# Kernel tuning notes

Hardware: AMD Instinct MI355X
Metric: run time of the kernel (lower is better)

Reference implementation:

```python
import jax, jax.numpy as jnp
import numpy as np

E = 16          # num_experts
TOP_K = 4       # num_experts_per_tok
H = 2048        # hidden_size
I_MOE = 1408    # moe_intermediate_size
I_SH = 5632     # shared_expert_intermediate_size
NORM_TOPK = False


def setup_inputs() -> dict:
    key = jax.random.key(0)
    ks = jax.random.split(key, 9)
    s = 0.02  # init scale
    return {
        "hidden_states": jax.random.normal(ks[0], (1, 1024, H), jnp.float32),
        "w_router": jax.random.normal(ks[1], (E, H), jnp.float32) * s,        # gate.weight [E,H]
        "w_gate": jax.random.normal(ks[2], (E, I_MOE, H), jnp.float32) * s,   # per-expert gate_proj.weight
        "w_up": jax.random.normal(ks[3], (E, I_MOE, H), jnp.float32) * s,     # per-expert up_proj.weight
        "w_down": jax.random.normal(ks[4], (E, H, I_MOE), jnp.float32) * s,   # per-expert down_proj.weight
        "ws_gate": jax.random.normal(ks[5], (I_SH, H), jnp.float32) * s,      # shared expert gate_proj
        "ws_up": jax.random.normal(ks[6], (I_SH, H), jnp.float32) * s,        # shared expert up_proj
        "ws_down": jax.random.normal(ks[7], (H, I_SH), jnp.float32) * s,      # shared expert down_proj
        "w_shared_gate": jax.random.normal(ks[8], (1, H), jnp.float32) * s,   # shared_expert_gate.weight
    }


def reference(hidden_states, w_router, w_gate, w_up, w_down,
              ws_gate, ws_up, ws_down, w_shared_gate):
    B, S, Hd = hidden_states.shape
    x = hidden_states.reshape(-1, Hd)                       # [T,H]
    T = x.shape[0]

    # router
    router_logits = x @ w_router.T                          # [T,E]
    probs = jax.nn.softmax(router_logits.astype(jnp.float32), axis=-1)
    topk_w, topk_idx = jax.lax.top_k(probs, TOP_K)          # [T,K]
    if NORM_TOPK:
        topk_w = topk_w / topk_w.sum(axis=-1, keepdims=True)
    topk_w = topk_w.astype(x.dtype)

    # dense combine weights: comb[t,e] = routing weight of expert e for token t (0 if unselected)
    comb = jnp.zeros((T, E), x.dtype).at[jnp.arange(T)[:, None], topk_idx].add(topk_w)

    # experts: SiLU-gated MLP, weighted combine (zero weight => no contribution)
    g = jax.nn.silu(jnp.einsum('th,eih->eti', x, w_gate)) * jnp.einsum('th,eih->eti', x, w_up)  # [E,T,I]
    moe_out = jnp.einsum('eti,ehi,te->th', g, w_down, comb)  # [T,H]

    # shared expert with sigmoid gate
    sh = (jax.nn.silu(x @ ws_gate.T) * (x @ ws_up.T)) @ ws_down.T   # [T,H]
    sh = jax.nn.sigmoid(x @ w_shared_gate.T) * sh

    final = (moe_out + sh).reshape(B, S, Hd)
    return final, router_logits
```

## Files before the change

kernel.cpp:

```cpp
#include <hip/hip_runtime.h>
#include <hip/hip_bf16.h>
#include <cmath>

#define TT   1024
#define HH   2048
#define EE   16
#define KTOP 4
#define IM   1408
#define ISHD 5632
#define BK   64

typedef __bf16 bf16x8 __attribute__((ext_vector_type(8)));
typedef __bf16 bf16x4 __attribute__((ext_vector_type(4)));
typedef float  f32x4  __attribute__((ext_vector_type(4)));

__device__ inline bf16x4 cvt4(float4 f) {
    bf16x4 r;
    r[0] = (__bf16)f.x; r[1] = (__bf16)f.y; r[2] = (__bf16)f.z; r[3] = (__bf16)f.w;
    return r;
}

__device__ inline void lds_dma16(void* lds, const void* g) {
    __builtin_amdgcn_global_load_lds(
        (const __attribute__((address_space(1))) unsigned int*)g,
        (__attribute__((address_space(3))) unsigned int*)lds, 16, 0, 0);
}

__global__ __launch_bounds__(256) void cvtx_kernel(
    const float* __restrict__ x, __bf16* __restrict__ xb) {
    const int i = (blockIdx.x * 256 + threadIdx.x) * 4;
    *(bf16x4*)(xb + i) = cvt4(*(const float4*)(x + i));
}

__global__ __launch_bounds__(256) void router_kernel(
    const float* __restrict__ x, const float* __restrict__ wr,
    const float* __restrict__ wshg,
    float* __restrict__ out_logits, int* __restrict__ counts,
    int* __restrict__ topk_e, int* __restrict__ topk_slot,
    float* __restrict__ topk_w, float* __restrict__ sgate)
{
    const int t    = blockIdx.x;
    const int tid  = threadIdx.x;
    const int wave = tid >> 6;
    const int lane = tid & 63;

    __shared__ float logits[EE];
    __shared__ float sgv;

    const float* xrow = x + (size_t)t * HH;
    float4 xv[4][2];
#pragma unroll
    for (int c = 0; c < 4; c++) {
        xv[c][0] = *(const float4*)(xrow + c * 512 + lane * 8);
        xv[c][1] = *(const float4*)(xrow + c * 512 + lane * 8 + 4);
    }

#pragma unroll
    for (int j = 0; j < 4; j++) {
        const int e = wave * 4 + j;
        const float* wrow = wr + (size_t)e * HH;
        float s = 0.f;
#pragma unroll
        for (int c = 0; c < 4; c++) {
            float4 w0 = *(const float4*)(wrow + c * 512 + lane * 8);
            float4 w1 = *(const float4*)(wrow + c * 512 + lane * 8 + 4);
            s += xv[c][0].x * w0.x + xv[c][0].y * w0.y + xv[c][0].z * w0.z + xv[c][0].w * w0.w;
            s += xv[c][1].x * w1.x + xv[c][1].y * w1.y + xv[c][1].z * w1.z + xv[c][1].w * w1.w;
        }
        for (int off = 32; off > 0; off >>= 1) s += __shfl_down(s, off, 64);
        if (lane == 0) logits[e] = s;
    }
    if (wave == 0) {
        float s = 0.f;
#pragma unroll
        for (int c = 0; c < 4; c++) {
            float4 w0 = *(const float4*)(wshg + c * 512 + lane * 8);
            float4 w1 = *(const float4*)(wshg + c * 512 + lane * 8 + 4);
            s += xv[c][0].x * w0.x + xv[c][0].y * w0.y + xv[c][0].z * w0.z + xv[c][0].w * w0.w;
            s += xv[c][1].x * w1.x + xv[c][1].y * w1.y + xv[c][1].z * w1.z + xv[c][1].w * w1.w;
        }
        for (int off = 32; off > 0; off >>= 1) s += __shfl_down(s, off, 64);
        if (lane == 0) sgv = s;
    }
    __syncthreads();

    if (tid == 0) {
        float mx = -1e30f;
        for (int e = 0; e < EE; e++) {
            out_logits[t * EE + e] = logits[e];
            mx = fmaxf(mx, logits[e]);
        }
        float p[EE]; float den = 0.f;
        for (int e = 0; e < EE; e++) { p[e] = expf(logits[e] - mx); den += p[e]; }
        const float inv = 1.f / den;
        bool used[EE];
        for (int e = 0; e < EE; e++) used[e] = false;
        for (int k = 0; k < KTOP; k++) {
            int best = 0; float bv = -1.f;
            for (int e = 0; e < EE; e++)
                if (!used[e] && p[e] > bv) { bv = p[e]; best = e; }
            used[best] = true;
            int slot = atomicAdd(&counts[best], 1);
            topk_e[t * KTOP + k]    = best;
            topk_slot[t * KTOP + k] = slot;
            topk_w[t * KTOP + k]    = bv * inv;
        }
        sgate[t] = 1.f / (1.f + expf(-sgv));
    }
}

__global__ void scan_kernel(const int* __restrict__ counts,
                            int* __restrict__ offsets) {
    if (threadIdx.x == 0 && blockIdx.x == 0) {
        int a = 0;
        for (int e = 0; e < EE; e++) { offsets[e] = a; a += counts[e]; }
        offsets[EE] = a;
    }
}

__global__ __launch_bounds__(256) void scatter_kernel(
    const int* __restrict__ offsets, const int* __restrict__ topk_e,
    const int* __restrict__ topk_slot, const float* __restrict__ topk_w,
    int* __restrict__ tok_list, float* __restrict__ wlist)
{
    const int i = blockIdx.x * 256 + threadIdx.x;
    if (i < TT * KTOP) {
        const int e   = topk_e[i];
        const int pos = offsets[e] + topk_slot[i];
        tok_list[pos] = i >> 2;
        wlist[pos]    = topk_w[i];
    }
}

__global__ __launch_bounds__(256) void gateup_kernel(
    const __bf16* __restrict__ xb, const float* __restrict__ wgate,
    const float* __restrict__ wup, const int* __restrict__ counts,
    const int* __restrict__ offsets, const int* __restrict__ tok_list,
    const float* __restrict__ wlist, __bf16* __restrict__ Gout, const int I)
{
    const int e    = blockIdx.z;
    const int Ne   = counts ? counts[e]  : TT;
    const int base = counts ? offsets[e] : 0;
    const int m0 = blockIdx.y * 128;
    if (m0 >= Ne) return;
    const int n0 = blockIdx.x * 64;

    __shared__ __bf16 As[2][128][64];
    __shared__ __bf16 Bgs[2][64][64];
    __shared__ __bf16 Bus[2][64][64];

    const int tid  = threadIdx.x;
    const int wave = tid >> 6, lane = tid & 63;

    const int arw = lane >> 3;
    const int sc8 = ((lane & 7) ^ arw) * 8;
    const __bf16* agp[4];
#pragma unroll
    for (int p = 0; p < 4; p++) {
        const int row = p * 32 + wave * 8 + arw;
        const int sc  = min(m0 + row, Ne - 1);
        const int tok = tok_list ? tok_list[base + sc] : sc;
        agp[p] = xb + (size_t)tok * HH + sc8;
    }

    const int brow = tid >> 4;
    const int bc4  = tid & 15;
    const float* bgptr[4];
    const float* buptr[4];
#pragma unroll
    for (int p = 0; p < 4; p++) {
        const size_t off = ((size_t)e * I + n0 + p * 16 + brow) * HH + bc4 * 4;
        bgptr[p] = wgate + off;
        buptr[p] = wup   + off;
    }
    const int bwo = ((((bc4 >> 1) ^ (brow & 7)) << 3) | ((bc4 & 1) << 2));

    const int wm = wave >> 1, wn = wave & 1;
    const int q = lane >> 4, r = lane & 15;
    const int r7 = r & 7;

    f32x4 accg[4][2], accu[4][2];
#pragma unroll
    for (int i = 0; i < 4; i++)
#pragma unroll
        for (int j = 0; j < 2; j++) {
            accg[i][j] = (f32x4){0.f, 0.f, 0.f, 0.f};
            accu[i][j] = (f32x4){0.f, 0.f, 0.f, 0.f};
        }

    float4 bgv[4], buv[4];

    auto loadB = [&](int kk) {
#pragma unroll
        for (int p = 0; p < 4; p++) {
            bgv[p] = *(const float4*)(bgptr[p] + kk);
            buv[p] = *(const float4*)(buptr[p] + kk);
        }
    };
    auto writeB = [&](int buf) {
#pragma unroll
        for (int p = 0; p < 4; p++) {
            *(bf16x4*)&Bgs[buf][p * 16 + brow][bwo] = cvt4(bgv[p]);
            *(bf16x4*)&Bus[buf][p * 16 + brow][bwo] = cvt4(buv[p]);
        }
    };
    auto issueA = [&](int buf, int kk) {
#pragma unroll
        for (int p = 0; p < 4; p++)
            lds_dma16(&As[buf][p * 32 + wave * 8][0], agp[p] + kk);
    };
    auto compute = [&](int buf) {
#pragma unroll
        for (int ks = 0; ks < BK; ks += 32) {
            const int cb = (ks >> 3) + q;
            bf16x8 af[4], bgf[2], buf2[2];
#pragma unroll
            for (int i = 0; i < 4; i++)
                af[i] = *(const bf16x8*)&As[buf][wm * 64 + i * 16 + r][(cb ^ r7) * 8];
#pragma unroll
            for (int j = 0; j < 2; j++) {
                bgf[j]  = *(const bf16x8*)&Bgs[buf][wn * 32 + j * 16 + r][(cb ^ r7) * 8];
                buf2[j] = *(const bf16x8*)&Bus[buf][wn * 32 + j * 16 + r][(cb ^ r7) * 8];
            }
#pragma unroll
            for (int i = 0; i < 4; i++)
#pragma unroll
                for (int j = 0; j < 2; j++) {
                    accg[i][j] = __builtin_amdgcn_mfma_f32_16x16x32_bf16(af[i], bgf[j],  accg[i][j], 0, 0, 0);
                    accu[i][j] = __builtin_amdgcn_mfma_f32_16x16x32_bf16(af[i], buf2[j], accu[i][j], 0, 0, 0);
                }
        }
    };

    constexpr int NS = HH / BK;
    loadB(0);
    issueA(0, 0);
    writeB(0);
    loadB(BK);
    for (int s = 0; s < NS; ++s) {
        __syncthreads();
        const int cur = s & 1;
        if (s + 1 < NS) {
            writeB(cur ^ 1);
            issueA(cur ^ 1, (s + 1) * BK);
            if (s + 2 < NS) loadB((s + 2) * BK);
        }
        compute(cur);
    }

#pragma unroll
    for (int i = 0; i < 4; i++)
#pragma unroll
        for (int reg = 0; reg < 4; reg++) {
            const int srow = m0 + wm * 64 + i * 16 + q * 4 + reg;
            if (srow < Ne) {
                const float w = wlist ? wlist[base + srow] : 1.f;
                __bf16* gp = Gout + (size_t)(base + srow) * I + n0 + wn * 32;
#pragma unroll
                for (int j = 0; j < 2; j++) {
                    float g = accg[i][j][reg];
                    float u = accu[i][j][reg];
                    float act = g / (1.f + expf(-g));
                    gp[j * 16 + r] = (__bf16)(act * u * w);
                }
            }
        }
}

__global__ __launch_bounds__(256) void down_kernel(
    const __bf16* __restrict__ G, const float* __restrict__ wd,
    const int* __restrict__ counts, const int* __restrict__ offsets,
    const int* __restrict__ tok_list, float* __restrict__ moeacc)
{
    const int e    = blockIdx.z;
    const int Ne   = counts[e];
    const int base = offsets[e];
    const int m0 = blockIdx.y * 128;
    if (m0 >= Ne) return;
    const int n0 = blockIdx.x * 128;

    __shared__ __bf16 As[2][128][64];
    __shared__ __bf16 Bs[2][128][64];

    const int tid  = threadIdx.x;
    const int wave = tid >> 6, lane = tid & 63;

    const int arw = lane >> 3;
    const int sc8 = ((lane & 7) ^ arw) * 8;
    const __bf16* agp[4];
#pragma unroll
    for (int p = 0; p < 4; p++) {
        const int row = p * 32 + wave * 8 + arw;
        const int sc  = min(m0 + row, Ne - 1);
        agp[p] = G + (size_t)(base + sc) * IM + sc8;
    }

    const int brow = tid >> 4;
    const int bc4  = tid & 15;
    const float* bptr[8];
#pragma unroll
    for (int p = 0; p < 8; p++)
        bptr[p] = wd + ((size_t)e * HH + n0 + p * 16 + brow) * IM + bc4 * 4;
    const int bwo = ((((bc4 >> 1) ^ (brow & 7)) << 3) | ((bc4 & 1) << 2));

    const int wm = wave >> 1, wn = wave & 1;
    const int q = lane >> 4, r = lane & 15;
    const int r7 = r & 7;

    f32x4 acc[4][4];
#pragma unroll
    for (int i = 0; i < 4; i++)
#pragma unroll
        for (int j = 0; j < 4; j++) acc[i][j] = (f32x4){0.f, 0.f, 0.f, 0.f};

    float4 bv[8];

    auto loadB = [&](int kk) {
#pragma unroll
        for (int p = 0; p < 8; p++) bv[p] = *(const float4*)(bptr[p] + kk);
    };
    auto writeB = [&](int buf) {
#pragma unroll
        for (int p = 0; p < 8; p++)
            *(bf16x4*)&Bs[buf][p * 16 + brow][bwo] = cvt4(bv[p]);
    };
    auto issueA = [&](int buf, int kk) {
#pragma unroll
        for (int p = 0; p < 4; p++)
            lds_dma16(&As[buf][p * 32 + wave * 8][0], agp[p] + kk);
    };
    auto compute = [&](int buf) {
#pragma unroll
        for (int ks = 0; ks < BK; ks += 32) {
            const int cb = (ks >> 3) + q;
            bf16x8 af[4], bf[4];
#pragma unroll
            for (int i = 0; i < 4; i++)
                af[i] = *(const bf16x8*)&As[buf][wm * 64 + i * 16 + r][(cb ^ r7) * 8];
#pragma unroll
            for (int j = 0; j < 4; j++)
                bf[j] = *(const bf16x8*)&Bs[buf][wn * 64 + j * 16 + r][(cb ^ r7) * 8];
#pragma unroll
            for (int i = 0; i < 4; i++)
#pragma unroll
                for (int j = 0; j < 4; j++)
                    acc[i][j] = __builtin_amdgcn_mfma_f32_16x16x32_bf16(af[i], bf[j], acc[i][j], 0, 0, 0);
        }
    };

    constexpr int NS = IM / BK;
    loadB(0);
    issueA(0, 0);
    writeB(0);
    loadB(BK);
    for (int s = 0; s < NS; ++s) {
        __syncthreads();
        const int cur = s & 1;
        if (s + 1 < NS) {
            writeB(cur ^ 1);
            issueA(cur ^ 1, (s + 1) * BK);
            if (s + 2 < NS) loadB((s + 2) * BK);
        }
        compute(cur);
    }

#pragma unroll
    for (int i = 0; i < 4; i++)
#pragma unroll
        for (int reg = 0; reg < 4; reg++) {
            const int srow = m0 + wm * 64 + i * 16 + q * 4 + reg;
            if (srow < Ne) {
                const int tok = tok_list[base + srow];
                float* mp = moeacc + (size_t)tok * HH + n0 + wn * 64;
#pragma unroll
                for (int j = 0; j < 4; j++)
                    atomicAdd(mp + j * 16 + r, acc[i][j][reg]);
            }
        }
}

__global__ __launch_bounds__(256) void shdown_kernel(
    const __bf16* __restrict__ S, const float* __restrict__ wsd,
    const float* __restrict__ moeacc, const float* __restrict__ sgate,
    float* __restrict__ out)
{
    const int m0 = blockIdx.y * 128;
    const int n0 = blockIdx.x * 64;

    __shared__ __bf16 As[2][128][64];
    __shared__ __bf16 Bs[2][64][64];

    const int tid  = threadIdx.x;
    const int wave = tid >> 6, lane = tid & 63;

    const int arw = lane >> 3;
    const int sc8 = ((lane & 7) ^ arw) * 8;
    const __bf16* agp[4];
#pragma unroll
    for (int p = 0; p < 4; p++) {
        const int row = p * 32 + wave * 8 + arw;
        agp[p] = S + (size_t)(m0 + row) * ISHD + sc8;
    }

    const int brow = tid >> 4;
    const int bc4  = tid & 15;
    const float* bptr[4];
#pragma unroll
    for (int p = 0; p < 4; p++)
        bptr[p] = wsd + (size_t)(n0 + p * 16 + brow) * ISHD + bc4 * 4;
    const int bwo = ((((bc4 >> 1) ^ (brow & 7)) << 3) | ((bc4 & 1) << 2));

    const int wm = wave >> 1, wn = wave & 1;
    const int q = lane >> 4, r = lane & 15;
    const int r7 = r & 15 & 7;

    f32x4 acc[4][2];
#pragma unroll
    for (int i = 0; i < 4; i++)
#pragma unroll
        for (int j = 0; j < 2; j++) acc[i][j] = (f32x4){0.f, 0.f, 0.f, 0.f};

    float4 bv[4];

    auto loadB = [&](int kk) {
#pragma unroll
        for (int p = 0; p < 4; p++) bv[p] = *(const float4*)(bptr[p] + kk);
    };
    auto writeB = [&](int buf) {
#pragma unroll
        for (int p = 0; p < 4; p++)
            *(bf16x4*)&Bs[buf][p * 16 + brow][bwo] = cvt4(bv[p]);
    };
    auto issueA = [&](int buf, int kk) {
#pragma unroll
        for (int p = 0; p < 4; p++)
            lds_dma16(&As[buf][p * 32 + wave * 8][0], agp[p] + kk);
    };
    auto compute = [&](int buf) {
#pragma unroll
        for (int ks = 0; ks < BK; ks += 32) {
            const int cb = (ks >> 3) + q;
            bf16x8 af[4], bf[2];
#pragma unroll
            for (int i = 0; i < 4; i++)
                af[i] = *(const bf16x8*)&As[buf][wm * 64 + i * 16 + r][(cb ^ r7) * 8];
#pragma unroll
            for (int j = 0; j < 2; j++)
                bf[j] = *(const bf16x8*)&Bs[buf][wn * 32 + j * 16 + r][(cb ^ r7) * 8];
#pragma unroll
            for (int i = 0; i < 4; i++)
#pragma unroll
                for (int j = 0; j < 2; j++)
                    acc[i][j] = __builtin_amdgcn_mfma_f32_16x16x32_bf16(af[i], bf[j], acc[i][j], 0, 0, 0);
        }
    };

    constexpr int NS = ISHD / BK;
    loadB(0);
    issueA(0, 0);
    writeB(0);
    loadB(BK);
    for (int s = 0; s < NS; ++s) {
        __syncthreads();
        const int cur = s & 1;
        if (s + 1 < NS) {
            writeB(cur ^ 1);
            issueA(cur ^ 1, (s + 1) * BK);
            if (s + 2 < NS) loadB((s + 2) * BK);
        }
        compute(cur);
    }

#pragma unroll
    for (int i = 0; i < 4; i++)
#pragma unroll
        for (int reg = 0; reg < 4; reg++) {
            const int t  = m0 + wm * 64 + i * 16 + q * 4 + reg;
            const float sg = sgate[t];
            const float* mp = moeacc + (size_t)t * HH + n0 + wn * 32;
            float* op = out + (size_t)t * HH + n0 + wn * 32;
#pragma unroll
            for (int j = 0; j < 2; j++)
                op[j * 16 + r] = mp[j * 16 + r] + sg * acc[i][j][reg];
        }
}

extern "C" void kernel_launch(void* const* d_in, const int* in_sizes, int n_in,
                              void* d_out, int out_size, void* d_ws, size_t ws_size,
                              hipStream_t stream) {
    const float* x    = (const float*)d_in[0];
    const float* wr   = (const float*)d_in[1];
    const float* wg   = (const float*)d_in[2];
    const float* wu   = (const float*)d_in[3];
    const float* wd   = (const float*)d_in[4];
    const float* wsg  = (const float*)d_in[5];
    const float* wsu  = (const float*)d_in[6];
    const float* wsd  = (const float*)d_in[7];
    const float* wshg = (const float*)d_in[8];

    float* out        = (float*)d_out;
    float* out_logits = out + (size_t)TT * HH;

    char* ws = (char*)d_ws;
    int*    counts    = (int*)(ws + 0);
    int*    offsets   = (int*)(ws + 256);
    int*    topk_e    = (int*)(ws + 512);
    int*    topk_slot = (int*)(ws + 512 + 16384);
    float*  topk_w    = (float*)(ws + 512 + 32768);
    float*  sgate     = (float*)(ws + 512 + 49152);
    int*    tok_list  = (int*)(ws + 512 + 53248);
    float*  wlist     = (float*)(ws + 512 + 69632);
    __bf16* xb        = (__bf16*)(ws + 86528);
    float*  moeacc    = (float*)(ws + 86528 + 4194304);
    char*   GS        = (char*)moeacc + (size_t)TT * HH * 4;
    __bf16* G = (__bf16*)GS;
    __bf16* S = (__bf16*)GS;

    hipMemsetAsync(counts, 0, EE * sizeof(int), stream);
    hipMemsetAsync(moeacc, 0, (size_t)TT * HH * sizeof(float), stream);

    cvtx_kernel<<<TT * HH / 1024, 256, 0, stream>>>(x, xb);
    router_kernel<<<TT, 256, 0, stream>>>(x, wr, wshg, out_logits,
                                          counts, topk_e, topk_slot, topk_w, sgate);
    scan_kernel<<<1, 64, 0, stream>>>(counts, offsets);
    scatter_kernel<<<(TT * KTOP + 255) / 256, 256, 0, stream>>>(
        offsets, topk_e, topk_slot, topk_w, tok_list, wlist);

    gateup_kernel<<<dim3(IM / 64, TT / 128, EE), 256, 0, stream>>>(
        xb, wg, wu, counts, offsets, tok_list, wlist, G, IM);

    down_kernel<<<dim3(HH / 128, TT / 128, EE), 256, 0, stream>>>(
        G, wd, counts, offsets, tok_list, moeacc);

    gateup_kernel<<<dim3(ISHD / 64, TT / 128, 1), 256, 0, stream>>>(
        xb, wsg, wsu, nullptr, nullptr, nullptr, nullptr, S, ISHD);

    shdown_kernel<<<dim3(HH / 64, TT / 128, 1), 256, 0, stream>>>(
        S, wsd, moeacc, sgate, out);
}
```

Before: 996.3 us.

## Remap workgroups XCD-aware and deepen B-prefetch pipeline with explicit waitcnt barriers

Switches all four GEMM kernels to a 1D grid and remaps block IDs so that consecutive workgroups dispatched round-robin across the 8 XCDs land on neighbouring tiles. M-tiles of one N-tile share a chip's L2, which improves weight reuse. It also unrolls the main loop by two with two register sets of fp32 B prefetch, keeping loads two stages ahead. __syncthreads is replaced with manual s_waitcnt vmcnt plus s_barrier. The risks are more register pressure and fragile hand-counted vmcnt values that must match the number of outstanding loads.

```diff
diff --git a/kernel.cpp b/kernel.cpp
--- a/kernel.cpp
+++ b/kernel.cpp
@@ -25,6 +25,9 @@
         (const __attribute__((address_space(1))) unsigned int*)g,
         (__attribute__((address_space(3))) unsigned int*)lds, 16, 0, 0);
 }
+
+#define WAITCNT(vm) asm volatile("s_waitcnt vmcnt(" #vm ") lgkmcnt(0)" ::: "memory")
+#define BARRIER() do { __builtin_amdgcn_s_barrier(); __builtin_amdgcn_sched_barrier(0); } while (0)
 
 __global__ __launch_bounds__(256) void cvtx_kernel(
     const float* __restrict__ x, __bf16* __restrict__ xb) {
@@ -138,12 +141,21 @@
     const int* __restrict__ offsets, const int* __restrict__ tok_list,
     const float* __restrict__ wlist, __bf16* __restrict__ Gout, const int I)
 {
-    const int e    = blockIdx.z;
+    const int nwg   = gridDim.x;
+    const int chunk = nwg >> 3;
+    const int bid   = blockIdx.x;
+    const int orig  = (bid & 7) * chunk + (bid >> 3);
+    const int mt    = orig & 7;
+    const int rest  = orig >> 3;
+    const int NX    = I >> 6;
+    const int nt    = rest % NX;
+    const int e     = rest / NX;
+
     const int Ne   = counts ? counts[e]  : TT;
     const int base = counts ? offsets[e] : 0;
-    const int m0 = blockIdx.y * 128;
+    const int m0 = mt * 128;
     if (m0 >= Ne) return;
-    const int n0 = blockIdx.x * 64;
+    const int n0 = nt * 64;
 
     __shared__ __bf16 As[2][128][64];
     __shared__ __bf16 Bgs[2][64][64];
@@ -188,20 +200,34 @@
             accu[i][j] = (f32x4){0.f, 0.f, 0.f, 0.f};
         }
 
-    float4 bgv[4], buv[4];
-
-    auto loadB = [&](int kk) {
+    float4 bgv0[4], buv0[4], bgv1[4], buv1[4];
+
+    auto loadB0 = [&](int kk) {
 #pragma unroll
         for (int p = 0; p < 4; p++) {
-            bgv[p] = *(const float4*)(bgptr[p] + kk);
-            buv[p] = *(const float4*)(buptr[p] + kk);
-        }
-    };
-    auto writeB = [&](int buf) {
+            bgv0[p] = *(const float4*)(bgptr[p] + kk);
+            buv0[p] = *(const float4*)(buptr[p] + kk);
+        }
+    };
+    auto loadB1 = [&](int kk) {
 #pragma unroll
         for (int p = 0; p < 4; p++) {
-            *(bf16x4*)&Bgs[buf][p * 16 + brow][bwo] = cvt4(bgv[p]);
-            *(bf16x4*)&Bus[buf][p * 16 + brow][bwo] = cvt4(buv[p]);
+            bgv1[p] = *(const float4*)(bgptr[p] + kk);
+            buv1[p] = *(const float4*)(buptr[p] + kk);
+        }
+    };
+    auto writeB0 = [&](int buf) {
+#pragma unroll
+        for (int p = 0; p < 4; p++) {
+            *(bf16x4*)&Bgs[buf][p * 16 + brow][bwo] = cvt4(bgv0[p]);
+            *(bf16x4*)&Bus[buf][p * 16 + brow][bwo] = cvt4(buv0[p]);
+        }
+    };
+    auto writeB1 = [&](int buf) {
+#pragma unroll
+        for (int p = 0; p < 4; p++) {
+            *(bf16x4*)&Bgs[buf][p * 16 + brow][bwo] = cvt4(bgv1[p]);
+            *(bf16x4*)&Bus[buf][p * 16 + brow][bwo] = cvt4(buv1[p]);
         }
     };
     auto issueA = [&](int buf, int kk) {
@@ -233,19 +259,29 @@
     };
 
     constexpr int NS = HH / BK;
-    loadB(0);
-    issueA(0, 0);
-    writeB(0);
-    loadB(BK);
-    for (int s = 0; s < NS; ++s) {
-        __syncthreads();
-        const int cur = s & 1;
+    loadB0(0); issueA(0, 0);
+    writeB0(0);
+    loadB1(BK);
+    loadB0(2 * BK);
+    WAITCNT(16);
+    BARRIER();
+
+#pragma unroll 1
+    for (int s = 0; s < NS; s += 2) {
+        if (s + 1 < NS) { writeB1(1); issueA(1, (s + 1) * BK); }
+        if (s + 3 < NS) loadB1((s + 3) * BK);
+        compute(0);
         if (s + 1 < NS) {
-            writeB(cur ^ 1);
-            issueA(cur ^ 1, (s + 1) * BK);
-            if (s + 2 < NS) loadB((s + 2) * BK);
-        }
-        compute(cur);
+            if (s + 3 < NS) WAITCNT(8); else WAITCNT(0);
+            BARRIER();
+            if (s + 2 < NS) { writeB0(0); issueA(0, (s + 2) * BK); }
+            if (s + 4 < NS) loadB0((s + 4) * BK);
+            compute(1);
+            if (s + 2 < NS) {
+                if (s + 4 < NS) WAITCNT(8); else WAITCNT(0);
+                BARRIER();
+            }
+        }
     }
 
 #pragma unroll
@@ -272,12 +308,20 @@
     const int* __restrict__ counts, const int* __restrict__ offsets,
     const int* __restrict__ tok_list, float* __restrict__ moeacc)
 {
-    const int e    = blockIdx.z;
+    const int nwg   = gridDim.x;
+    const int chunk = nwg >> 3;
+    const int bid   = blockIdx.x;
+    const int orig  = (bid & 7) * chunk + (bid >> 3);
+    const int mt    = orig & 7;
+    const int rest  = orig >> 3;
+    const int nt    = rest & 15;
+    const int e     = rest >> 4;
+
     const int Ne   = counts[e];
     const int base = offsets[e];
-    const int m0 = blockIdx.y * 128;
+    const int m0 = mt * 128;
     if (m0 >= Ne) return;
-    const int n0 = blockIdx.x * 128;
+    const int n0 = nt * 128;
 
     __shared__ __bf16 As[2][128][64];
     __shared__ __bf16 Bs[2][128][64];
@@ -313,16 +357,25 @@
 #pragma unroll
         for (int j = 0; j < 4; j++) acc[i][j] = (f32x4){0.f, 0.f, 0.f, 0.f};
 
-    float4 bv[8];
-
-    auto loadB = [&](int kk) {
-#pragma unroll
-        for (int p = 0; p < 8; p++) bv[p] = *(const float4*)(bptr[p] + kk);
-    };
-    auto writeB = [&](int buf) {
+    float4 bv0[8], bv1[8];
+
+    auto loadB0 = [&](int kk) {
+#pragma unroll
+        for (int p = 0; p < 8; p++) bv0[p] = *(const float4*)(bptr[p] + kk);
+    };
+    auto loadB1 = [&](int kk) {
+#pragma unroll
+        for (int p = 0; p < 8; p++) bv1[p] = *(const float4*)(bptr[p] + kk);
+    };
+    auto writeB0 = [&](int buf) {
 #pragma unroll
         for (int p = 0; p < 8; p++)
-            *(bf16x4*)&Bs[buf][p * 16 + brow][bwo] = cvt4(bv[p]);
+            *(bf16x4*)&Bs[buf][p * 16 + brow][bwo] = cvt4(bv0[p]);
+    };
+    auto writeB1 = [&](int buf) {
+#pragma unroll
+        for (int p = 0; p < 8; p++)
+            *(bf16x4*)&Bs[buf][p * 16 + brow][bwo] = cvt4(bv1[p]);
     };
     auto issueA = [&](int buf, int kk) {
 #pragma unroll
@@ -349,19 +402,29 @@
     };
 
     constexpr int NS = IM / BK;
-    loadB(0);
-    issueA(0, 0);
-    writeB(0);
-    loadB(BK);
-    for (int s = 0; s < NS; ++s) {
-        __syncthreads();
-        const int cur = s & 1;
+    loadB0(0); issueA(0, 0);
+    writeB0(0);
+    loadB1(BK);
+    loadB0(2 * BK);
+    WAITCNT(16);
+    BARRIER();
+
+#pragma unroll 1
+    for (int s = 0; s < NS; s += 2) {
+        if (s + 1 < NS) { writeB1(1); issueA(1, (s + 1) * BK); }
+        if (s + 3 < NS) loadB1((s + 3) * BK);
+        compute(0);
         if (s + 1 < NS) {
-            writeB(cur ^ 1);
-            issueA(cur ^ 1, (s + 1) * BK);
-            if (s + 2 < NS) loadB((s + 2) * BK);
-        }
-        compute(cur);
+            if (s + 3 < NS) WAITCNT(8); else WAITCNT(0);
+            BARRIER();
+            if (s + 2 < NS) { writeB0(0); issueA(0, (s + 2) * BK); }
+            if (s + 4 < NS) loadB0((s + 4) * BK);
+            compute(1);
+            if (s + 2 < NS) {
+                if (s + 4 < NS) WAITCNT(8); else WAITCNT(0);
+                BARRIER();
+            }
+        }
     }
 
 #pragma unroll
@@ -384,8 +447,15 @@
     const float* __restrict__ moeacc, const float* __restrict__ sgate,
     float* __restrict__ out)
 {
-    const int m0 = blockIdx.y * 128;
-    const int n0 = blockIdx.x * 64;
+    const int nwg   = gridDim.x;
+    const int chunk = nwg >> 3;
+    const int bid   = blockIdx.x;
+    const int orig  = (bid & 7) * chunk + (bid >> 3);
+    const int mt    = orig & 7;
+    const int nt    = orig >> 3;
+
+    const int m0 = mt * 128;
+    const int n0 = nt * 64;
 
     __shared__ __bf16 As[2][128][64];
     __shared__ __bf16 Bs[2][64][64];
@@ -412,7 +482,7 @@
 
     const int wm = wave >> 1, wn = wave & 1;
     const int q = lane >> 4, r = lane & 15;
-    const int r7 = r & 15 & 7;
+    const int r7 = r & 7;
 
     f32x4 acc[4][2];
 #pragma unroll
@@ -420,16 +490,25 @@
 #pragma unroll
         for (int j = 0; j < 2; j++) acc[i][j] = (f32x4){0.f, 0.f, 0.f, 0.f};
 
-    float4 bv[4];
-
-    auto loadB = [&](int kk) {
-#pragma unroll
-        for (int p = 0; p < 4; p++) bv[p] = *(const float4*)(bptr[p] + kk);
-    };
-    auto writeB = [&](int buf) {
+    float4 bv0[4], bv1[4];
+
+    auto loadB0 = [&](int kk) {
+#pragma unroll
+        for (int p = 0; p < 4; p++) bv0[p] = *(const float4*)(bptr[p] + kk);
+    };
+    auto loadB1 = [&](int kk) {
+#pragma unroll
+        for (int p = 0; p < 4; p++) bv1[p] = *(const float4*)(bptr[p] + kk);
+    };
+    auto writeB0 = [&](int buf) {
 #pragma unroll
         for (int p = 0; p < 4; p++)
-            *(bf16x4*)&Bs[buf][p * 16 + brow][bwo] = cvt4(bv[p]);
+            *(bf16x4*)&Bs[buf][p * 16 + brow][bwo] = cvt4(bv0[p]);
+    };
+    auto writeB1 = [&](int buf) {
+#pragma unroll
+        for (int p = 0; p < 4; p++)
+            *(bf16x4*)&Bs[buf][p * 16 + brow][bwo] = cvt4(bv1[p]);
     };
     auto issueA = [&](int buf, int kk) {
 #pragma unroll
@@ -456,19 +535,29 @@
     };
 
     constexpr int NS = ISHD / BK;
-    loadB(0);
-    issueA(0, 0);
-    writeB(0);
-    loadB(BK);
-    for (int s = 0; s < NS; ++s) {
-        __syncthreads();
-        const int cur = s & 1;
+    loadB0(0); issueA(0, 0);
+    writeB0(0);
+    loadB1(BK);
+    loadB0(2 * BK);
+    WAITCNT(8);
+    BARRIER();
+
+#pragma unroll 1
+    for (int s = 0; s < NS; s += 2) {
+        if (s + 1 < NS) { writeB1(1); issueA(1, (s + 1) * BK); }
+        if (s + 3 < NS) loadB1((s + 3) * BK);
+        compute(0);
         if (s + 1 < NS) {
-            writeB(cur ^ 1);
-            issueA(cur ^ 1, (s + 1) * BK);
-            if (s + 2 < NS) loadB((s + 2) * BK);
-        }
-        compute(cur);
+            if (s + 3 < NS) WAITCNT(4); else WAITCNT(0);
+            BARRIER();
+            if (s + 2 < NS) { writeB0(0); issueA(0, (s + 2) * BK); }
+            if (s + 4 < NS) loadB0((s + 4) * BK);
+            compute(1);
+            if (s + 2 < NS) {
+                if (s + 4 < NS) WAITCNT(4); else WAITCNT(0);
+                BARRIER();
+            }
+        }
     }
 
 #pragma unroll
@@ -526,15 +615,15 @@
     scatter_kernel<<<(TT * KTOP + 255) / 256, 256, 0, stream>>>(
         offsets, topk_e, topk_slot, topk_w, tok_list, wlist);
 
-    gateup_kernel<<<dim3(IM / 64, TT / 128, EE), 256, 0, stream>>>(
+    gateup_kernel<<<dim3(8 * (IM / 64) * EE), 256, 0, stream>>>(
         xb, wg, wu, counts, offsets, tok_list, wlist, G, IM);
 
-    down_kernel<<<dim3(HH / 128, TT / 128, EE), 256, 0, stream>>>(
+    down_kernel<<<dim3(8 * (HH / 128) * EE), 256, 0, stream>>>(
         G, wd, counts, offsets, tok_list, moeacc);
 
-    gateup_kernel<<<dim3(ISHD / 64, TT / 128, 1), 256, 0, stream>>>(
+    gateup_kernel<<<dim3(8 * (ISHD / 64)), 256, 0, stream>>>(
         xb, wsg, wsu, nullptr, nullptr, nullptr, nullptr, S, ISHD);
 
-    shdown_kernel<<<dim3(HH / 64, TT / 128, 1), 256, 0, stream>>>(
+    shdown_kernel<<<dim3(8 * (HH / 64)), 256, 0, stream>>>(
         S, wsd, moeacc, sgate, out);
 }
```

Result: slower. 1.114 ms (+11.8%).

## Use XCD-aware 1D block remap and register-staged single-buffer LDS tiles

Applied to the files above, without the earlier changes.

Replaces the 3D grids with a 1D grid whose block index is remapped across the 8 XCDs so that the M-tiles sharing one weight N-tile land on the same XCD and can reuse its L2. The double-buffered LDS pipeline with global_load_lds DMA and XOR swizzle is replaced by a single padded LDS buffer (row stride 72) filled from registers, with the next K-slice prefetched into registers during compute. This trades the async DMA overlap and double buffering for two barriers per K step and simpler, padded bank-conflict avoidance, with lower LDS use per block.

```diff
diff --git a/kernel.cpp b/kernel.cpp
--- a/kernel.cpp
+++ b/kernel.cpp
@@ -18,12 +18,6 @@
     bf16x4 r;
     r[0] = (__bf16)f.x; r[1] = (__bf16)f.y; r[2] = (__bf16)f.z; r[3] = (__bf16)f.w;
     return r;
-}
-
-__device__ inline void lds_dma16(void* lds, const void* g) {
-    __builtin_amdgcn_global_load_lds(
-        (const __attribute__((address_space(1))) unsigned int*)g,
-        (__attribute__((address_space(3))) unsigned int*)lds, 16, 0, 0);
 }
 
 __global__ __launch_bounds__(256) void cvtx_kernel(
@@ -138,46 +132,50 @@
     const int* __restrict__ offsets, const int* __restrict__ tok_list,
     const float* __restrict__ wlist, __bf16* __restrict__ Gout, const int I)
 {
-    const int e    = blockIdx.z;
+    const int nwg   = gridDim.x;
+    const int chunk = nwg >> 3;
+    const int bid   = blockIdx.x;
+    const int orig  = (bid & 7) * chunk + (bid >> 3);
+    const int mt    = orig & 7;
+    const int rest  = orig >> 3;
+    const int NX    = I >> 6;
+    const int nt    = rest % NX;
+    const int e     = rest / NX;
+
     const int Ne   = counts ? counts[e]  : TT;
     const int base = counts ? offsets[e] : 0;
-    const int m0 = blockIdx.y * 128;
+    const int m0 = mt * 128;
     if (m0 >= Ne) return;
-    const int n0 = blockIdx.x * 64;
-
-    __shared__ __bf16 As[2][128][64];
-    __shared__ __bf16 Bgs[2][64][64];
-    __shared__ __bf16 Bus[2][64][64];
-
-    const int tid  = threadIdx.x;
-    const int wave = tid >> 6, lane = tid & 63;
-
-    const int arw = lane >> 3;
-    const int sc8 = ((lane & 7) ^ arw) * 8;
-    const __bf16* agp[4];
+    const int n0 = nt * 64;
+
+    __shared__ __bf16 As[128][72];
+    __shared__ __bf16 Bgs[64][72];
+    __shared__ __bf16 Bus[64][72];
+
+    const int tid = threadIdx.x;
+    const int arow = tid >> 3;
+    const int acg  = tid & 7;
+    const __bf16* aptr[4];
 #pragma unroll
     for (int p = 0; p < 4; p++) {
-        const int row = p * 32 + wave * 8 + arw;
-        const int sc  = min(m0 + row, Ne - 1);
-        const int tok = tok_list ? tok_list[base + sc] : sc;
-        agp[p] = xb + (size_t)tok * HH + sc8;
-    }
-
+        int sc  = min(m0 + p * 32 + arow, Ne - 1);
+        int tok = tok_list ? tok_list[base + sc] : sc;
+        aptr[p] = xb + (size_t)tok * HH + acg * 8;
+    }
     const int brow = tid >> 4;
     const int bc4  = tid & 15;
     const float* bgptr[4];
     const float* buptr[4];
 #pragma unroll
     for (int p = 0; p < 4; p++) {
-        const size_t off = ((size_t)e * I + n0 + p * 16 + brow) * HH + bc4 * 4;
+        size_t off = ((size_t)e * I + n0 + p * 16 + brow) * HH + bc4 * 4;
         bgptr[p] = wgate + off;
         buptr[p] = wup   + off;
     }
-    const int bwo = ((((bc4 >> 1) ^ (brow & 7)) << 3) | ((bc4 & 1) << 2));
-
+
+    const int wave = tid >> 6, lane = tid & 63;
     const int wm = wave >> 1, wn = wave & 1;
     const int q = lane >> 4, r = lane & 15;
-    const int r7 = r & 7;
 
     f32x4 accg[4][2], accu[4][2];
 #pragma unroll
@@ -188,64 +186,51 @@
             accu[i][j] = (f32x4){0.f, 0.f, 0.f, 0.f};
         }
 
-    float4 bgv[4], buv[4];
-
-    auto loadB = [&](int kk) {
+    bf16x8 av[4]; float4 bgv[4], buv[4];
+#pragma unroll
+    for (int p = 0; p < 4; p++) {
+        av[p]  = *(const bf16x8*)(aptr[p]);
+        bgv[p] = *(const float4*)(bgptr[p]);
+        buv[p] = *(const float4*)(buptr[p]);
+    }
+
+    for (int kk = 0; kk < HH; kk += BK) {
+        __syncthreads();
 #pragma unroll
         for (int p = 0; p < 4; p++) {
-            bgv[p] = *(const float4*)(bgptr[p] + kk);
-            buv[p] = *(const float4*)(buptr[p] + kk);
-        }
-    };
-    auto writeB = [&](int buf) {
-#pragma unroll
-        for (int p = 0; p < 4; p++) {
-            *(bf16x4*)&Bgs[buf][p * 16 + brow][bwo] = cvt4(bgv[p]);
-            *(bf16x4*)&Bus[buf][p * 16 + brow][bwo] = cvt4(buv[p]);
-        }
-    };
-    auto issueA = [&](int buf, int kk) {
-#pragma unroll
-        for (int p = 0; p < 4; p++)
-            lds_dma16(&As[buf][p * 32 + wave * 8][0], agp[p] + kk);
-    };
-    auto compute = [&](int buf) {
+            *(bf16x8*)&As[p * 32 + arow][acg * 8]  = av[p];
+            *(bf16x4*)&Bgs[p * 16 + brow][bc4 * 4] = cvt4(bgv[p]);
+            *(bf16x4*)&Bus[p * 16 + brow][bc4 * 4] = cvt4(buv[p]);
+        }
+        __syncthreads();
+        if (kk + BK < HH) {
+            const int ko = kk + BK;
+#pragma unroll
+            for (int p = 0; p < 4; p++) {
+                av[p]  = *(const bf16x8*)(aptr[p] + ko);
+                bgv[p] = *(const float4*)(bgptr[p] + ko);
+                buv[p] = *(const float4*)(buptr[p] + ko);
+            }
+        }
 #pragma unroll
         for (int ks = 0; ks < BK; ks += 32) {
-            const int cb = (ks >> 3) + q;
-            bf16x8 af[4], bgf[2], buf2[2];
+            bf16x8 af[4], bgf[2], buf[2];
 #pragma unroll
             for (int i = 0; i < 4; i++)
-                af[i] = *(const bf16x8*)&As[buf][wm * 64 + i * 16 + r][(cb ^ r7) * 8];
+                af[i] = *(const bf16x8*)&As[wm * 64 + i * 16 + r][ks + q * 8];
 #pragma unroll
             for (int j = 0; j < 2; j++) {
-                bgf[j]  = *(const bf16x8*)&Bgs[buf][wn * 32 + j * 16 + r][(cb ^ r7) * 8];
-                buf2[j] = *(const bf16x8*)&Bus[buf][wn * 32 + j * 16 + r][(cb ^ r7) * 8];
+                bgf[j] = *(const bf16x8*)&Bgs[wn * 32 + j * 16 + r][ks + q * 8];
+                buf[j] = *(const bf16x8*)&Bus[wn * 32 + j * 16 + r][ks + q * 8];
             }
 #pragma unroll
             for (int i = 0; i < 4; i++)
 #pragma unroll
                 for (int j = 0; j < 2; j++) {
-                    accg[i][j] = __builtin_amdgcn_mfma_f32_16x16x32_bf16(af[i], bgf[j],  accg[i][j], 0, 0, 0);
-                    accu[i][j] = __builtin_amdgcn_mfma_f32_16x16x32_bf16(af[i], buf2[j], accu[i][j], 0, 0, 0);
+                    accg[i][j] = __builtin_amdgcn_mfma_f32_16x16x32_bf16(af[i], bgf[j], accg[i][j], 0, 0, 0);
+                    accu[i][j] = __builtin_amdgcn_mfma_f32_16x16x32_bf16(af[i], buf[j], accu[i][j], 0, 0, 0);
                 }
         }
-    };
-
-    constexpr int NS = HH / BK;
-    loadB(0);
-    issueA(0, 0);
-    writeB(0);
-    loadB(BK);
-    for (int s = 0; s < NS; ++s) {
-        __syncthreads();
-        const int cur = s & 1;
-        if (s + 1 < NS) {
-            writeB(cur ^ 1);
-            issueA(cur ^ 1, (s + 1) * BK);
-            if (s + 2 < NS) loadB((s + 2) * BK);
-        }
-        compute(cur);
     }
 
 #pragma unroll
@@ -272,40 +257,43 @@
     const int* __restrict__ counts, const int* __restrict__ offsets,
     const int* __restrict__ tok_list, float* __restrict__ moeacc)
 {
-    const int e    = blockIdx.z;
+    const int nwg   = gridDim.x;
+    const int chunk = nwg >> 3;
+    const int bid   = blockIdx.x;
+    const int orig  = (bid & 7) * chunk + (bid >> 3);
+    const int mt    = orig & 7;
+    const int rest  = orig >> 3;
+    const int nt    = rest & 15;
+    const int e     = rest >> 4;
+
     const int Ne   = counts[e];
     const int base = offsets[e];
-    const int m0 = blockIdx.y * 128;
+    const int m0 = mt * 128;
     if (m0 >= Ne) return;
-    const int n0 = blockIdx.x * 128;
-
-    __shared__ __bf16 As[2][128][64];
-    __shared__ __bf16 Bs[2][128][64];
-
-    const int tid  = threadIdx.x;
-    const int wave = tid >> 6, lane = tid & 63;
-
-    const int arw = lane >> 3;
-    const int sc8 = ((lane & 7) ^ arw) * 8;
-    const __bf16* agp[4];
+    const int n0 = nt * 128;
+
+    __shared__ __bf16 As[128][72];
+    __shared__ __bf16 Bs[128][72];
+
+    const int tid = threadIdx.x;
+    const int arow = tid >> 3;
+    const int acg  = tid & 7;
+    const __bf16* aptr[4];
 #pragma unroll
     for (int p = 0; p < 4; p++) {
-        const int row = p * 32 + wave * 8 + arw;
-        const int sc  = min(m0 + row, Ne - 1);
-        agp[p] = G + (size_t)(base + sc) * IM + sc8;
-    }
-
+        int sc = min(m0 + p * 32 + arow, Ne - 1);
+        aptr[p] = G + (size_t)(base + sc) * IM + acg * 8;
+    }
     const int brow = tid >> 4;
     const int bc4  = tid & 15;
     const float* bptr[8];
 #pragma unroll
     for (int p = 0; p < 8; p++)
         bptr[p] = wd + ((size_t)e * HH + n0 + p * 16 + brow) * IM + bc4 * 4;
-    const int bwo = ((((bc4 >> 1) ^ (brow & 7)) << 3) | ((bc4 & 1) << 2));
-
+
+    const int wave = tid >> 6, lane = tid & 63;
     const int wm = wave >> 1, wn = wave & 1;
     const int q = lane >> 4, r = lane & 15;
-    const int r7 = r & 7;
 
     f32x4 acc[4][4];
 #pragma unroll
@@ -313,55 +301,43 @@
 #pragma unroll
         for (int j = 0; j < 4; j++) acc[i][j] = (f32x4){0.f, 0.f, 0.f, 0.f};
 
-    float4 bv[8];
-
-    auto loadB = [&](int kk) {
-#pragma unroll
-        for (int p = 0; p < 8; p++) bv[p] = *(const float4*)(bptr[p] + kk);
-    };
-    auto writeB = [&](int buf) {
+    bf16x8 av[4]; float4 bv[8];
+#pragma unroll
+    for (int p = 0; p < 4; p++) av[p] = *(const bf16x8*)(aptr[p]);
+#pragma unroll
+    for (int p = 0; p < 8; p++) bv[p] = *(const float4*)(bptr[p]);
+
+    for (int kk = 0; kk < IM; kk += BK) {
+        __syncthreads();
+#pragma unroll
+        for (int p = 0; p < 4; p++)
+            *(bf16x8*)&As[p * 32 + arow][acg * 8] = av[p];
 #pragma unroll
         for (int p = 0; p < 8; p++)
-            *(bf16x4*)&Bs[buf][p * 16 + brow][bwo] = cvt4(bv[p]);
-    };
-    auto issueA = [&](int buf, int kk) {
-#pragma unroll
-        for (int p = 0; p < 4; p++)
-            lds_dma16(&As[buf][p * 32 + wave * 8][0], agp[p] + kk);
-    };
-    auto compute = [&](int buf) {
+            *(bf16x4*)&Bs[p * 16 + brow][bc4 * 4] = cvt4(bv[p]);
+        __syncthreads();
+        if (kk + BK < IM) {
+            const int ko = kk + BK;
+#pragma unroll
+            for (int p = 0; p < 4; p++) av[p] = *(const bf16x8*)(aptr[p] + ko);
+#pragma unroll
+            for (int p = 0; p < 8; p++) bv[p] = *(const float4*)(bptr[p] + ko);
+        }
 #pragma unroll
         for (int ks = 0; ks < BK; ks += 32) {
-            const int cb = (ks >> 3) + q;
             bf16x8 af[4], bf[4];
 #pragma unroll
             for (int i = 0; i < 4; i++)
-                af[i] = *(const bf16x8*)&As[buf][wm * 64 + i * 16 + r][(cb ^ r7) * 8];
+                af[i] = *(const bf16x8*)&As[wm * 64 + i * 16 + r][ks + q * 8];
 #pragma unroll
             for (int j = 0; j < 4; j++)
-                bf[j] = *(const bf16x8*)&Bs[buf][wn * 64 + j * 16 + r][(cb ^ r7) * 8];
+                bf[j] = *(const bf16x8*)&Bs[wn * 64 + j * 16 + r][ks + q * 8];
 #pragma unroll
             for (int i = 0; i < 4; i++)
 #pragma unroll
                 for (int j = 0; j < 4; j++)
                     acc[i][j] = __builtin_amdgcn_mfma_f32_16x16x32_bf16(af[i], bf[j], acc[i][j], 0, 0, 0);
         }
-    };
-
-    constexpr int NS = IM / BK;
-    loadB(0);
-    issueA(0, 0);
-    writeB(0);
-    loadB(BK);
-    for (int s = 0; s < NS; ++s) {
-        __syncthreads();
-        const int cur = s & 1;
-        if (s + 1 < NS) {
-            writeB(cur ^ 1);
-            issueA(cur ^ 1, (s + 1) * BK);
-            if (s + 2 < NS) loadB((s + 2) * BK);
-        }
-        compute(cur);
     }
 
 #pragma unroll
@@ -384,35 +360,36 @@
     const float* __restrict__ moeacc, const float* __restrict__ sgate,
     float* __restrict__ out)
 {
-    const int m0 = blockIdx.y * 128;
-    const int n0 = blockIdx.x * 64;
-
-    __shared__ __bf16 As[2][128][64];
-    __shared__ __bf16 Bs[2][64][64];
-
-    const int tid  = threadIdx.x;
-    const int wave = tid >> 6, lane = tid & 63;
-
-    const int arw = lane >> 3;
-    const int sc8 = ((lane & 7) ^ arw) * 8;
-    const __bf16* agp[4];
-#pragma unroll
-    for (int p = 0; p < 4; p++) {
-        const int row = p * 32 + wave * 8 + arw;
-        agp[p] = S + (size_t)(m0 + row) * ISHD + sc8;
-    }
-
+    const int nwg   = gridDim.x;
+    const int chunk = nwg >> 3;
+    const int bid   = blockIdx.x;
+    const int orig  = (bid & 7) * chunk + (bid >> 3);
+    const int mt    = orig & 7;
+    const int nt    = orig >> 3;
+
+    const int m0 = mt * 128;
+    const int n0 = nt * 64;
+
+    __shared__ __bf16 As[128][72];
+    __shared__ __bf16 Bs[64][72];
+
+    const int tid = threadIdx.x;
+    const int arow = tid >> 3;
+    const int acg  = tid & 7;
+    const __bf16* aptr[4];
+#pragma unroll
+    for (int p = 0; p < 4; p++)
+        aptr[p] = S + (size_t)(m0 + p * 32 + arow) * ISHD + acg * 8;
     const int brow = tid >> 4;
     const int bc4  = tid & 15;
     const float* bptr[4];
 #pragma unroll
     for (int p = 0; p < 4; p++)
         bptr[p] = wsd + (size_t)(n0 + p * 16 + brow) * ISHD + bc4 * 4;
-    const int bwo = ((((bc4 >> 1) ^ (brow & 7)) << 3) | ((bc4 & 1) << 2));
-
+
+    const int wave = tid >> 6, lane = tid & 63;
     const int wm = wave >> 1, wn = wave & 1;
     const int q = lane >> 4, r = lane & 15;
-    const int r7 = r & 15 & 7;
 
     f32x4 acc[4][2];
 #pragma unroll
@@ -420,55 +397,44 @@
 #pragma unroll
         for (int j = 0; j < 2; j++) acc[i][j] = (f32x4){0.f, 0.f, 0.f, 0.f};
 
-    float4 bv[4];
-
-    auto loadB = [&](int kk) {
-#pragma unroll
-        for (int p = 0; p < 4; p++) bv[p] = *(const float4*)(bptr[p] + kk);
-    };
-    auto writeB = [&](int buf) {
-#pragma unroll
-        for (int p = 0; p < 4; p++)
-            *(bf16x4*)&Bs[buf][p * 16 + brow][bwo] = cvt4(bv[p]);
-    };
-    auto issueA = [&](int buf, int kk) {
-#pragma unroll
-        for (int p = 0; p < 4; p++)
-            lds_dma16(&As[buf][p * 32 + wave * 8][0], agp[p] + kk);
-    };
-    auto compute = [&](int buf) {
+    bf16x8 av[4]; float4 bv[4];
+#pragma unroll
+    for (int p = 0; p < 4; p++) {
+        av[p] = *(const bf16x8*)(aptr[p]);
+        bv[p] = *(const float4*)(bptr[p]);
+    }
+
+    for (int kk = 0; kk < ISHD; kk += BK) {
+        __syncthreads();
+#pragma unroll
+        for (int p = 0; p < 4; p++) {
+            *(bf16x8*)&As[p * 32 + arow][acg * 8]  = av[p];
+            *(bf16x4*)&Bs[p * 16 + brow][bc4 * 4] = cvt4(bv[p]);
+        }
+        __syncthreads();
+        if (kk + BK < ISHD) {
+            const int ko = kk + BK;
+#pragma unroll
+            for (int p = 0; p < 4; p++) {
+                av[p] = *(const bf16x8*)(aptr[p] + ko);
+                bv[p] = *(const float4*)(bptr[p] + ko);
+            }
+        }
 #pragma unroll
         for (int ks = 0; ks < BK; ks += 32) {
-            const int cb = (ks >> 3) + q;
             bf16x8 af[4], bf[2];
 #pragma unroll
             for (int i = 0; i < 4; i++)
-                af[i] = *(const bf16x8*)&As[buf][wm * 64 + i * 16 + r][(cb ^ r7) * 8];
+                af[i] = *(const bf16x8*)&As[wm * 64 + i * 16 + r][ks + q * 8];
 #pragma unroll
             for (int j = 0; j < 2; j++)
-                bf[j] = *(const bf16x8*)&Bs[buf][wn * 32 + j * 16 + r][(cb ^ r7) * 8];
+                bf[j] = *(const bf16x8*)&Bs[wn * 32 + j * 16 + r][ks + q * 8];
 #pragma unroll
             for (int i = 0; i < 4; i++)
 #pragma unroll
                 for (int j = 0; j < 2; j++)
                     acc[i][j] = __builtin_amdgcn_mfma_f32_16x16x32_bf16(af[i], bf[j], acc[i][j], 0, 0, 0);
         }
-    };
-
-    constexpr int NS = ISHD / BK;
-    loadB(0);
-    issueA(0, 0);
-    writeB(0);
-    loadB(BK);
-    for (int s = 0; s < NS; ++s) {
-        __syncthreads();
-        const int cur = s & 1;
-        if (s + 1 < NS) {
-            writeB(cur ^ 1);
-            issueA(cur ^ 1, (s + 1) * BK);
-            if (s + 2 < NS) loadB((s + 2) * BK);
-        }
-        compute(cur);
     }
 
 #pragma unroll
@@ -526,15 +492,15 @@
     scatter_kernel<<<(TT * KTOP + 255) / 256, 256, 0, stream>>>(
         offsets, topk_e, topk_slot, topk_w, tok_list, wlist);
 
-    gateup_kernel<<<dim3(IM / 64, TT / 128, EE), 256, 0, stream>>>(
+    gateup_kernel<<<dim3(8 * (IM / 64) * EE), 256, 0, stream>>>(
         xb, wg, wu, counts, offsets, tok_list, wlist, G, IM);
 
-    down_kernel<<<dim3(HH / 128, TT / 128, EE), 256, 0, stream>>>(
+    down_kernel<<<dim3(8 * (HH / 128) * EE), 256, 0, stream>>>(
         G, wd, counts, offsets, tok_list, moeacc);
 
-    gateup_kernel<<<dim3(ISHD / 64, TT / 128, 1), 256, 0, stream>>>(
+    gateup_kernel<<<dim3(8 * (ISHD / 64)), 256, 0, stream>>>(
         xb, wsg, wsu, nullptr, nullptr, nullptr, nullptr, S, ISHD);
 
-    shdown_kernel<<<dim3(HH / 64, TT / 128, 1), 256, 0, stream>>>(
+    shdown_kernel<<<dim3(8 * (HH / 64)), 256, 0, stream>>>(
         S, wsd, moeacc, sgate, out);
 }
```

Result: faster. 914.2 us (-8.2%).
